# Kernel optimization log

Measured on AMD Instinct MI355X. Metric: run time of the kernel, lower is better.

## Reference

```python
import jax, jax.numpy as jnp
import numpy as np

N_NODES = 50000
N_EDGES = 800000
D_IN = 128
D_HID = 16
N_CLS = 3


def setup_inputs() -> dict:
    key = jax.random.key(0)
    k = jax.random.split(key, 8)
    x = jax.random.normal(k[0], (N_NODES, D_IN), dtype=jnp.float32)
    edge_index = jax.random.randint(k[1], (2, N_EDGES), 0, N_NODES, dtype=jnp.int64)
    # SAGEConv params: lin_l (applied to aggregated neighbors, has bias),
    # lin_r (applied to root node, no bias) -- PyG defaults with mean aggregation.
    s1 = 1.0 / np.sqrt(D_IN)
    s2 = 1.0 / np.sqrt(D_HID)
    W1_l = jax.random.normal(k[2], (D_HID, D_IN), dtype=jnp.float32) * s1
    b1_l = jnp.zeros((D_HID,), dtype=jnp.float32)
    W1_r = jax.random.normal(k[3], (D_HID, D_IN), dtype=jnp.float32) * s1
    W2_l = jax.random.normal(k[4], (N_CLS, D_HID), dtype=jnp.float32) * s2
    b2_l = jnp.zeros((N_CLS,), dtype=jnp.float32)
    W2_r = jax.random.normal(k[5], (N_CLS, D_HID), dtype=jnp.float32) * s2
    return {"x": x, "edge_index": edge_index, "W1_l": W1_l, "b1_l": b1_l,
            "W1_r": W1_r, "W2_l": W2_l, "b2_l": b2_l, "W2_r": W2_r}


def _mean_aggregate(x, src, dst, num_nodes):
    # messages x_j = x[src] scattered to dst, mean-reduced (PyG SAGEConv aggr='mean')
    summed = jax.ops.segment_sum(x[src], dst, num_segments=num_nodes)  # [N, D]
    counts = jax.ops.segment_sum(jnp.ones((src.shape[0],), dtype=x.dtype), dst,
                                 num_segments=num_nodes)
    return summed / jnp.maximum(counts, 1.0)[:, None]


def _sage_conv(x, src, dst, W_l, b_l, W_r, num_nodes):
    agg = _mean_aggregate(x, src, dst, num_nodes)
    return agg @ W_l.T + b_l + x @ W_r.T


def reference(x, edge_index, W1_l, b1_l, W1_r, W2_l, b2_l, W2_r):
    src, dst = edge_index[0], edge_index[1]
    n = x.shape[0]
    h = jax.nn.relu(_sage_conv(x, src, dst, W1_l, b1_l, W1_r, n))
    h = jax.nn.relu(_sage_conv(h, src, dst, W2_l, b2_l, W2_r, n))
    return jax.nn.log_softmax(h, axis=1)
```

## Files before the change

### kernel.cpp

```cpp
#include <hip/hip_runtime.h>
#include <math.h>

#define D_IN 128
#define D_HID 16
#define N_CLS 3
#define NXCD 8

__global__ __launch_bounds__(128) void lin1_kernel(
    const float* __restrict__ x, const float* __restrict__ W1l,
    const float* __restrict__ W1r, float* __restrict__ y_l,
    float* __restrict__ y_r, int n_nodes)
{
    __shared__ float xs[64 * 132];
    __shared__ float ws[32 * 132];
    const int t = threadIdx.x;
    const int node0 = blockIdx.x * 64;

    for (int m = t; m < (32 * 128) / 4; m += 128) {
        int f = m * 4;
        int row = f >> 7, col = f & 127;
        const float* srcw = (row < 16) ? (W1l + row * 128 + col)
                                       : (W1r + (row - 16) * 128 + col);
        float4 g = *(const float4*)srcw;
        *(float4*)&ws[row * 132 + col] = g;
    }
    for (int m = t; m < (64 * 128) / 4; m += 128) {
        int f = m * 4;
        int row = f >> 7, col = f & 127;
        int node = node0 + row;
        float4 g = make_float4(0.f, 0.f, 0.f, 0.f);
        if (node < n_nodes) g = *(const float4*)(x + (size_t)node * D_IN + col);
        *(float4*)&xs[row * 132 + col] = g;
    }
    __syncthreads();

    const int ng = t >> 3;
    const int og = t & 7;
    float acc[4][4];
    #pragma unroll
    for (int i = 0; i < 4; ++i)
        #pragma unroll
        for (int j = 0; j < 4; ++j) acc[i][j] = 0.f;

    for (int k = 0; k < 128; k += 4) {
        float4 xv[4], wv[4];
        #pragma unroll
        for (int i = 0; i < 4; ++i)
            xv[i] = *(const float4*)&xs[(ng + 16 * i) * 132 + k];
        #pragma unroll
        for (int j = 0; j < 4; ++j)
            wv[j] = *(const float4*)&ws[(og + 8 * j) * 132 + k];
        #pragma unroll
        for (int i = 0; i < 4; ++i)
            #pragma unroll
            for (int j = 0; j < 4; ++j) {
                acc[i][j] = fmaf(xv[i].x, wv[j].x, acc[i][j]);
                acc[i][j] = fmaf(xv[i].y, wv[j].y, acc[i][j]);
                acc[i][j] = fmaf(xv[i].z, wv[j].z, acc[i][j]);
                acc[i][j] = fmaf(xv[i].w, wv[j].w, acc[i][j]);
            }
    }

    #pragma unroll
    for (int i = 0; i < 4; ++i) {
        int node = node0 + ng + 16 * i;
        if (node >= n_nodes) continue;
        #pragma unroll
        for (int j = 0; j < 4; ++j) {
            int col = og + 8 * j;
            if (col < 16) y_l[(size_t)node * 16 + col] = acc[i][j];
            else          y_r[(size_t)node * 16 + (col - 16)] = acc[i][j];
        }
    }
}


__global__ __launch_bounds__(256) void fillx_kernel(
    const int* __restrict__ src, const int* __restrict__ dst,
    int* __restrict__ deg, int* __restrict__ padadj,
    int n_edges, int cap, int n8, int n_nodes, int bpx)
{
    const int x  = blockIdx.x & (NXCD - 1);
    const int q  = blockIdx.x >> 3;
    const int lo = x * n8;
    int hi = lo + n8; if (hi > n_nodes) hi = n_nodes;
    const int stride = bpx * 256;

    const int e4n = n_edges >> 2;
    for (int i = q * 256 + threadIdx.x; i < e4n; i += stride) {
        int4 d4 = *(const int4*)&dst[i * 4];
        if (d4.x >= lo && d4.x < hi) {
            int r = atomicAdd(&deg[d4.x], 1);
            if (r < cap) padadj[(size_t)d4.x * cap + r] = src[i * 4 + 0];
        }
        if (d4.y >= lo && d4.y < hi) {
            int r = atomicAdd(&deg[d4.y], 1);
            if (r < cap) padadj[(size_t)d4.y * cap + r] = src[i * 4 + 1];
        }
        if (d4.z >= lo && d4.z < hi) {
            int r = atomicAdd(&deg[d4.z], 1);
            if (r < cap) padadj[(size_t)d4.z * cap + r] = src[i * 4 + 2];
        }
        if (d4.w >= lo && d4.w < hi) {
            int r = atomicAdd(&deg[d4.w], 1);
            if (r < cap) padadj[(size_t)d4.w * cap + r] = src[i * 4 + 3];
        }
    }
    if (q == 0 && threadIdx.x < (n_edges & 3)) {
        int e = (e4n << 2) + threadIdx.x;
        int d = dst[e];
        if (d >= lo && d < hi) {
            int r = atomicAdd(&deg[d], 1);
            if (r < cap) padadj[(size_t)d * cap + r] = src[e];
        }
    }
}

__global__ __launch_bounds__(256) void gather1x_kernel(
    const int* __restrict__ deg, const int* __restrict__ padadj,
    const float* __restrict__ y_l, const float* __restrict__ y_r,
    const float* __restrict__ b1, const float* __restrict__ W2l,
    const float* __restrict__ W2r, float* __restrict__ z_l,
    float* __restrict__ z_r, int n_nodes, int cap, int n8)
{
    const int t = threadIdx.x;
    const int c = t & 15;
    const int x = blockIdx.x & (NXCD - 1);
    const int q = blockIdx.x >> 3;
    const int local = q * 16 + (t >> 4);
    if (local >= n8) return;
    const int n = x * n8 + local;
    if (n >= n_nodes) return;

    const int dc = deg[n];
    const int* ap = padadj + (size_t)n * cap;
    float acc = 0.f;
    int j = 0;
    for (; j + 4 <= dc; j += 4) {
        int4 s4 = *(const int4*)(ap + j);
        float a0 = y_l[(size_t)s4.x * 16 + c];
        float a1 = y_l[(size_t)s4.y * 16 + c];
        float a2 = y_l[(size_t)s4.z * 16 + c];
        float a3 = y_l[(size_t)s4.w * 16 + c];
        acc += (a0 + a1) + (a2 + a3);
    }
    for (; j < dc; ++j) acc += y_l[(size_t)ap[j] * 16 + c];

    float inv = 1.0f / fmaxf((float)dc, 1.0f);
    float h = fmaxf(fmaf(acc, inv, b1[c] + y_r[(size_t)n * 16 + c]), 0.f);

    float zl[N_CLS], zr[N_CLS];
    #pragma unroll
    for (int o = 0; o < N_CLS; ++o) {
        float pl = h * W2l[o * 16 + c];
        float pr = h * W2r[o * 16 + c];
        #pragma unroll
        for (int d = 1; d < 16; d <<= 1) {
            pl += __shfl_xor(pl, d, 64);
            pr += __shfl_xor(pr, d, 64);
        }
        zl[o] = pl; zr[o] = pr;
    }
    if (c == 0) {
        *(float4*)&z_l[(size_t)n * 4] = make_float4(zl[0], zl[1], zl[2], 0.f);
        *(float4*)&z_r[(size_t)n * 4] = make_float4(zr[0], zr[1], zr[2], 0.f);
    }
}

__global__ __launch_bounds__(256) void gather2x_out_kernel(
    const int* __restrict__ deg, const int* __restrict__ padadj,
    const float* __restrict__ z_l, const float* __restrict__ z_r,
    const float* __restrict__ b2, float* __restrict__ out,
    int n_nodes, int cap, int n8)
{
    const int x = blockIdx.x & (NXCD - 1);
    const int q = blockIdx.x >> 3;
    const int local = q * 256 + threadIdx.x;
    if (local >= n8) return;
    const int n = x * n8 + local;
    if (n >= n_nodes) return;

    const int dc = deg[n];
    const int* ap = padadj + (size_t)n * cap;
    float a0 = 0.f, a1 = 0.f, a2 = 0.f;
    int j = 0;
    for (; j + 4 <= dc; j += 4) {
        int4 s4 = *(const int4*)(ap + j);
        float4 v0 = *(const float4*)&z_l[(size_t)s4.x * 4];
        float4 v1 = *(const float4*)&z_l[(size_t)s4.y * 4];
        float4 v2 = *(const float4*)&z_l[(size_t)s4.z * 4];
        float4 v3 = *(const float4*)&z_l[(size_t)s4.w * 4];
        a0 += (v0.x + v1.x) + (v2.x + v3.x);
        a1 += (v0.y + v1.y) + (v2.y + v3.y);
        a2 += (v0.z + v1.z) + (v2.z + v3.z);
    }
    for (; j < dc; ++j) {
        float4 v = *(const float4*)&z_l[(size_t)ap[j] * 4];
        a0 += v.x; a1 += v.y; a2 += v.z;
    }
    float inv = 1.0f / fmaxf((float)dc, 1.0f);
    float4 r = *(const float4*)&z_r[(size_t)n * 4];
    float v0 = fmaxf(fmaf(a0, inv, b2[0] + r.x), 0.f);
    float v1 = fmaxf(fmaf(a1, inv, b2[1] + r.y), 0.f);
    float v2 = fmaxf(fmaf(a2, inv, b2[2] + r.z), 0.f);
    float m = fmaxf(fmaxf(v0, v1), v2);
    float s = expf(v0 - m) + expf(v1 - m) + expf(v2 - m);
    float lse = m + logf(s);
    out[(size_t)n * 3 + 0] = v0 - lse;
    out[(size_t)n * 3 + 1] = v1 - lse;
    out[(size_t)n * 3 + 2] = v2 - lse;
}


__global__ __launch_bounds__(256) void hist_kernel(
    const int* __restrict__ dst, int* __restrict__ deg, int n_edges)
{
    int e = blockIdx.x * 256 + threadIdx.x;
    if (e < n_edges) atomicAdd(&deg[dst[e]], 1);
}

__global__ __launch_bounds__(1024) void scan_a_kernel(
    const int* __restrict__ deg, int* __restrict__ off,
    int* __restrict__ cur, int* __restrict__ bsum, int n)
{
    __shared__ int s[1024];
    const int t = threadIdx.x;
    const int base = blockIdx.x * 4096 + t * 4;
    int4 v = make_int4(0, 0, 0, 0);
    if (base + 3 < n) {
        v = *(const int4*)&deg[base];
    } else {
        if (base + 0 < n) v.x = deg[base + 0];
        if (base + 1 < n) v.y = deg[base + 1];
        if (base + 2 < n) v.z = deg[base + 2];
        if (base + 3 < n) v.w = deg[base + 3];
    }
    int tsum = v.x + v.y + v.z + v.w;
    s[t] = tsum;
    __syncthreads();
    for (int d = 1; d < 1024; d <<= 1) {
        int u = (t >= d) ? s[t - d] : 0;
        __syncthreads();
        s[t] += u;
        __syncthreads();
    }
    if (t == 1023) bsum[blockIdx.x] = s[1023];
    int e0 = s[t] - tsum;
    int e1 = e0 + v.x, e2 = e1 + v.y, e3 = e2 + v.z;
    if (base + 3 < n) {
        *(int4*)&off[base] = make_int4(e0, e1, e2, e3);
        *(int4*)&cur[base] = make_int4(e0, e1, e2, e3);
    } else {
        if (base + 0 < n) { off[base + 0] = e0; cur[base + 0] = e0; }
        if (base + 1 < n) { off[base + 1] = e1; cur[base + 1] = e1; }
        if (base + 2 < n) { off[base + 2] = e2; cur[base + 2] = e2; }
        if (base + 3 < n) { off[base + 3] = e3; cur[base + 3] = e3; }
    }
}

__global__ __launch_bounds__(64) void scan_b_kernel(
    int* __restrict__ bsum, int* __restrict__ off, int nblk, int n)
{
    const int t = threadIdx.x;
    int v = (t < nblk) ? bsum[t] : 0;
    int own = v;
    #pragma unroll
    for (int d = 1; d < 64; d <<= 1) {
        int u = __shfl_up(v, d, 64);
        if (t >= d) v += u;
    }
    if (t < nblk) bsum[t] = v - own;
    if (t == 63) off[n] = v;
}

__global__ __launch_bounds__(256) void scan_c_kernel(
    const int* __restrict__ bsum, int* __restrict__ off,
    int* __restrict__ cur, int n)
{
    int i = blockIdx.x * 256 + threadIdx.x;
    if (i >= n) return;
    int b = bsum[i >> 12];
    off[i] += b;
    cur[i] += b;
}

__global__ __launch_bounds__(256) void fill_kernel(
    const int* __restrict__ src, const int* __restrict__ dst,
    int* __restrict__ cursor, int* __restrict__ adj, int n_edges)
{
    int e = blockIdx.x * 256 + threadIdx.x;
    if (e >= n_edges) return;
    int slot = atomicAdd(&cursor[dst[e]], 1);
    adj[slot] = src[e];
}

__global__ __launch_bounds__(256) void gather1_kernel(
    const int* __restrict__ off, const int* __restrict__ adj,
    const float* __restrict__ y_l, const float* __restrict__ y_r,
    const float* __restrict__ b1, const float* __restrict__ W2l,
    const float* __restrict__ W2r, float* __restrict__ z_l,
    float* __restrict__ z_r, int n_nodes)
{
    const int t = threadIdx.x;
    const int c = t & 15;
    const int n = blockIdx.x * 16 + (t >> 4);
    if (n >= n_nodes) return;
    const int beg = off[n], end = off[n + 1];
    float acc = 0.f;
    for (int j = beg; j < end; ++j) {
        int s = adj[j];
        acc += y_l[(size_t)s * 16 + c];
    }
    float inv = 1.0f / fmaxf((float)(end - beg), 1.0f);
    float h = fmaxf(fmaf(acc, inv, b1[c] + y_r[(size_t)n * 16 + c]), 0.f);

    float zl[N_CLS], zr[N_CLS];
    #pragma unroll
    for (int o = 0; o < N_CLS; ++o) {
        float pl = h * W2l[o * 16 + c];
        float pr = h * W2r[o * 16 + c];
        #pragma unroll
        for (int d = 1; d < 16; d <<= 1) {
            pl += __shfl_xor(pl, d, 64);
            pr += __shfl_xor(pr, d, 64);
        }
        zl[o] = pl; zr[o] = pr;
    }
    if (c == 0) {
        *(float4*)&z_l[(size_t)n * 4] = make_float4(zl[0], zl[1], zl[2], 0.f);
        *(float4*)&z_r[(size_t)n * 4] = make_float4(zr[0], zr[1], zr[2], 0.f);
    }
}

__global__ __launch_bounds__(256) void gather2_out_kernel(
    const int* __restrict__ off, const int* __restrict__ adj,
    const float* __restrict__ z_l, const float* __restrict__ z_r,
    const float* __restrict__ b2, float* __restrict__ out, int n_nodes)
{
    int n = blockIdx.x * 256 + threadIdx.x;
    if (n >= n_nodes) return;
    const int beg = off[n], end = off[n + 1];
    float a0 = 0.f, a1 = 0.f, a2 = 0.f;
    for (int j = beg; j < end; ++j) {
        int s = adj[j];
        float4 v = *(const float4*)&z_l[(size_t)s * 4];
        a0 += v.x; a1 += v.y; a2 += v.z;
    }
    float inv = 1.0f / fmaxf((float)(end - beg), 1.0f);
    float4 r = *(const float4*)&z_r[(size_t)n * 4];
    float v0 = fmaxf(fmaf(a0, inv, b2[0] + r.x), 0.f);
    float v1 = fmaxf(fmaf(a1, inv, b2[1] + r.y), 0.f);
    float v2 = fmaxf(fmaf(a2, inv, b2[2] + r.z), 0.f);
    float m = fmaxf(fmaxf(v0, v1), v2);
    float s = expf(v0 - m) + expf(v1 - m) + expf(v2 - m);
    float lse = m + logf(s);
    out[(size_t)n * 3 + 0] = v0 - lse;
    out[(size_t)n * 3 + 1] = v1 - lse;
    out[(size_t)n * 3 + 2] = v2 - lse;
}

extern "C" void kernel_launch(void* const* d_in, const int* in_sizes, int n_in,
                              void* d_out, int out_size, void* d_ws, size_t ws_size,
                              hipStream_t stream)
{
    const float* x   = (const float*)d_in[0];
    const int*   ei  = (const int*)d_in[1];
    const float* W1l = (const float*)d_in[2];
    const float* b1  = (const float*)d_in[3];
    const float* W1r = (const float*)d_in[4];
    const float* W2l = (const float*)d_in[5];
    const float* b2  = (const float*)d_in[6];
    const float* W2r = (const float*)d_in[7];

    const int N = in_sizes[0] / D_IN;
    const int E = in_sizes[1] / 2;
    const int* srcI = ei;
    const int* dstI = ei + E;

    float* fws  = (float*)d_ws;
    float* y_l  = fws;
    float* y_r  = y_l + (size_t)N * 16;
    float* z_l  = y_r + (size_t)N * 16;
    float* z_r  = z_l + (size_t)N * 4;
    int*   iws  = (int*)(z_r + (size_t)N * 4);

    const size_t base_bytes = 160ULL * N + 4ULL * N;
    int CAP = 0;
    if (ws_size >= base_bytes + 256ULL * N)      CAP = 64;
    else if (ws_size >= base_bytes + 192ULL * N) CAP = 48;

    lin1_kernel<<<(N + 63) / 64, 128, 0, stream>>>(x, W1l, W1r, y_l, y_r, N);

    if (CAP) {
        int* deg    = iws;
        int* padadj = deg + N;
        const int n8  = (N + NXCD - 1) / NXCD;
        const int bpx = 128;

        hipMemsetAsync(deg, 0, (size_t)N * sizeof(int), stream);
        fillx_kernel<<<NXCD * bpx, 256, 0, stream>>>(srcI, dstI, deg, padadj,
                                                     E, CAP, n8, N, bpx);
        const int g1b = (n8 + 15) / 16;
        gather1x_kernel<<<NXCD * g1b, 256, 0, stream>>>(deg, padadj, y_l, y_r,
                                                        b1, W2l, W2r,
                                                        z_l, z_r, N, CAP, n8);
        const int g2b = (n8 + 255) / 256;
        gather2x_out_kernel<<<NXCD * g2b, 256, 0, stream>>>(deg, padadj,
                                                            z_l, z_r, b2,
                                                            (float*)d_out, N, CAP, n8);
    } else {
        int* deg  = iws;
        int* off  = deg + N;
        int* cur  = off + N + 1;
        int* adj  = cur + N;
        int* bsum = adj + E;

        const int nblk = (N + 4095) >> 12;

        hipMemsetAsync(deg, 0, (size_t)N * sizeof(int), stream);
        hist_kernel<<<(E + 255) / 256, 256, 0, stream>>>(dstI, deg, E);
        scan_a_kernel<<<nblk, 1024, 0, stream>>>(deg, off, cur, bsum, N);
        scan_b_kernel<<<1, 64, 0, stream>>>(bsum, off, nblk, N);
        scan_c_kernel<<<(N + 255) / 256, 256, 0, stream>>>(bsum, off, cur, N);
        fill_kernel<<<(E + 255) / 256, 256, 0, stream>>>(srcI, dstI, cur, adj, E);
        gather1_kernel<<<(N + 15) / 16, 256, 0, stream>>>(off, adj, y_l, y_r, b1,
                                                          W2l, W2r, z_l, z_r, N);
        gather2_out_kernel<<<(N + 255) / 256, 256, 0, stream>>>(off, adj, z_l, z_r,
                                                                b2, (float*)d_out, N);
    }
}
```

Baseline: 97.64 us.

## Build CSR via per-block shared-memory histograms and XCD-partitioned placement

Replaces the padded-adjacency default path with an exact CSR build. Each block, partitioned by destination range per XCD, counts edges in a shared-memory histogram, and a column scan gives per-block offsets. Edges are then placed with shared atomics, and the gather kernels read compact CSR with int4-vectorized neighbor loads. This avoids global atomics and padded slots, at the cost of more kernel launches, a CB×N count buffer in workspace, and reading the edge list twice.

After: 98.55 us. About the same (+0.9%).

```diff
diff --git a/kernel.cpp b/kernel.cpp
--- a/kernel.cpp
+++ b/kernel.cpp
@@ -5,6 +5,9 @@
 #define D_HID 16
 #define N_CLS 3
 #define NXCD 8
+#define CB 64
+#define CT 512
+#define HMAX 8192
 
 __global__ __launch_bounds__(128) void lin1_kernel(
     const float* __restrict__ x, const float* __restrict__ W1l,
@@ -72,6 +75,266 @@
             else          y_r[(size_t)node * 16 + (col - 16)] = acc[i][j];
         }
     }
+}
+
+
+__global__ __launch_bounds__(CT) void count_kernel(
+    const int* __restrict__ dst, int* __restrict__ bcnt,
+    int e4n, int n_edges, int n8, int n_nodes, int N)
+{
+    __shared__ int hist[HMAX];
+    const int x = blockIdx.x & (NXCD - 1);
+    const int b = blockIdx.x >> 3;
+    const int lo = x * n8;
+    int hi = lo + n8; if (hi > n_nodes) hi = n_nodes;
+    const int nloc = hi - lo;
+
+    for (int k = threadIdx.x; k < nloc; k += CT) hist[k] = 0;
+    __syncthreads();
+
+    const int g = b * CT + threadIdx.x;
+    const int stride = CB * CT;
+    for (int i = g; i < e4n; i += stride) {
+        int4 d4 = *(const int4*)&dst[i * 4];
+        if (d4.x >= lo && d4.x < hi) atomicAdd(&hist[d4.x - lo], 1);
+        if (d4.y >= lo && d4.y < hi) atomicAdd(&hist[d4.y - lo], 1);
+        if (d4.z >= lo && d4.z < hi) atomicAdd(&hist[d4.z - lo], 1);
+        if (d4.w >= lo && d4.w < hi) atomicAdd(&hist[d4.w - lo], 1);
+    }
+    if (b == 0 && threadIdx.x < (n_edges & 3)) {
+        int e = (e4n << 2) + threadIdx.x;
+        int d = dst[e];
+        if (d >= lo && d < hi) atomicAdd(&hist[d - lo], 1);
+    }
+    __syncthreads();
+    for (int k = threadIdx.x; k < nloc; k += CT)
+        bcnt[(size_t)b * N + lo + k] = hist[k];
+}
+
+__global__ __launch_bounds__(256) void colscan_kernel(
+    int* __restrict__ bcnt, int* __restrict__ deg, int n, int N)
+{
+    int d = blockIdx.x * 256 + threadIdx.x;
+    if (d >= n) return;
+    int s = 0;
+    #pragma unroll 4
+    for (int b = 0; b < CB; ++b) {
+        size_t idx = (size_t)b * N + d;
+        int t = bcnt[idx];
+        bcnt[idx] = s;
+        s += t;
+    }
+    deg[d] = s;
+}
+
+__global__ __launch_bounds__(1024) void scan_a_kernel(
+    const int* __restrict__ deg, int* __restrict__ off,
+    int* __restrict__ bsum, int n)
+{
+    __shared__ int s[1024];
+    const int t = threadIdx.x;
+    const int base = blockIdx.x * 4096 + t * 4;
+    int4 v = make_int4(0, 0, 0, 0);
+    if (base + 3 < n) {
+        v = *(const int4*)&deg[base];
+    } else {
+        if (base + 0 < n) v.x = deg[base + 0];
+        if (base + 1 < n) v.y = deg[base + 1];
+        if (base + 2 < n) v.z = deg[base + 2];
+        if (base + 3 < n) v.w = deg[base + 3];
+    }
+    int tsum = v.x + v.y + v.z + v.w;
+    s[t] = tsum;
+    __syncthreads();
+    for (int d = 1; d < 1024; d <<= 1) {
+        int u = (t >= d) ? s[t - d] : 0;
+        __syncthreads();
+        s[t] += u;
+        __syncthreads();
+    }
+    if (t == 1023) bsum[blockIdx.x] = s[1023];
+    int e0 = s[t] - tsum;
+    int e1 = e0 + v.x, e2 = e1 + v.y, e3 = e2 + v.z;
+    if (base + 3 < n) {
+        *(int4*)&off[base] = make_int4(e0, e1, e2, e3);
+    } else {
+        if (base + 0 < n) off[base + 0] = e0;
+        if (base + 1 < n) off[base + 1] = e1;
+        if (base + 2 < n) off[base + 2] = e2;
+        if (base + 3 < n) off[base + 3] = e3;
+    }
+}
+
+__global__ __launch_bounds__(64) void scan_b_kernel(
+    int* __restrict__ bsum, int* __restrict__ off, int nblk, int n)
+{
+    const int t = threadIdx.x;
+    int v = (t < nblk) ? bsum[t] : 0;
+    int own = v;
+    #pragma unroll
+    for (int d = 1; d < 64; d <<= 1) {
+        int u = __shfl_up(v, d, 64);
+        if (t >= d) v += u;
+    }
+    if (t < nblk) bsum[t] = v - own;
+    if (t == 63) off[n] = v;
+}
+
+__global__ __launch_bounds__(256) void scan_c_kernel(
+    const int* __restrict__ bsum, int* __restrict__ off, int n)
+{
+    int i = blockIdx.x * 256 + threadIdx.x;
+    if (i >= n) return;
+    off[i] += bsum[i >> 12];
+}
+
+__global__ __launch_bounds__(CT) void place_kernel(
+    const int* __restrict__ src, const int* __restrict__ dst,
+    const int* __restrict__ off, const int* __restrict__ bcnt,
+    int* __restrict__ adj, int e4n, int n_edges, int n8, int n_nodes, int N)
+{
+    __shared__ int cur[HMAX];
+    const int x = blockIdx.x & (NXCD - 1);
+    const int b = blockIdx.x >> 3;
+    const int lo = x * n8;
+    int hi = lo + n8; if (hi > n_nodes) hi = n_nodes;
+    const int nloc = hi - lo;
+
+    for (int k = threadIdx.x; k < nloc; k += CT)
+        cur[k] = off[lo + k] + bcnt[(size_t)b * N + lo + k];
+    __syncthreads();
+
+    const int g = b * CT + threadIdx.x;
+    const int stride = CB * CT;
+    for (int i = g; i < e4n; i += stride) {
+        int4 d4 = *(const int4*)&dst[i * 4];
+        if (d4.x >= lo && d4.x < hi) {
+            int p = atomicAdd(&cur[d4.x - lo], 1);
+            adj[p] = src[i * 4 + 0];
+        }
+        if (d4.y >= lo && d4.y < hi) {
+            int p = atomicAdd(&cur[d4.y - lo], 1);
+            adj[p] = src[i * 4 + 1];
+        }
+        if (d4.z >= lo && d4.z < hi) {
+            int p = atomicAdd(&cur[d4.z - lo], 1);
+            adj[p] = src[i * 4 + 2];
+        }
+        if (d4.w >= lo && d4.w < hi) {
+            int p = atomicAdd(&cur[d4.w - lo], 1);
+            adj[p] = src[i * 4 + 3];
+        }
+    }
+    if (b == 0 && threadIdx.x < (n_edges & 3)) {
+        int e = (e4n << 2) + threadIdx.x;
+        int d = dst[e];
+        if (d >= lo && d < hi) {
+            int p = atomicAdd(&cur[d - lo], 1);
+            adj[p] = src[e];
+        }
+    }
+}
+
+__global__ __launch_bounds__(256) void gather1c_kernel(
+    const int* __restrict__ off, const int* __restrict__ adj,
+    const float* __restrict__ y_l, const float* __restrict__ y_r,
+    const float* __restrict__ b1, const float* __restrict__ W2l,
+    const float* __restrict__ W2r, float* __restrict__ z_l,
+    float* __restrict__ z_r, int n_nodes, int n8)
+{
+    const int t = threadIdx.x;
+    const int c = t & 15;
+    const int x = blockIdx.x & (NXCD - 1);
+    const int q = blockIdx.x >> 3;
+    const int local = q * 16 + (t >> 4);
+    if (local >= n8) return;
+    const int n = x * n8 + local;
+    if (n >= n_nodes) return;
+
+    const int beg = off[n], end = off[n + 1];
+    float acc = 0.f;
+    int j = beg;
+    int alim = (beg + 3) & ~3;
+    if (alim > end) alim = end;
+    for (; j < alim; ++j) acc += y_l[(size_t)adj[j] * 16 + c];
+    for (; j + 4 <= end; j += 4) {
+        int4 s4 = *(const int4*)&adj[j];
+        float a0 = y_l[(size_t)s4.x * 16 + c];
+        float a1 = y_l[(size_t)s4.y * 16 + c];
+        float a2 = y_l[(size_t)s4.z * 16 + c];
+        float a3 = y_l[(size_t)s4.w * 16 + c];
+        acc += (a0 + a1) + (a2 + a3);
+    }
+    for (; j < end; ++j) acc += y_l[(size_t)adj[j] * 16 + c];
+
+    float inv = 1.0f / fmaxf((float)(end - beg), 1.0f);
+    float h = fmaxf(fmaf(acc, inv, b1[c] + y_r[(size_t)n * 16 + c]), 0.f);
+
+    float zl[N_CLS], zr[N_CLS];
+    #pragma unroll
+    for (int o = 0; o < N_CLS; ++o) {
+        float pl = h * W2l[o * 16 + c];
+        float pr = h * W2r[o * 16 + c];
+        #pragma unroll
+        for (int d = 1; d < 16; d <<= 1) {
+            pl += __shfl_xor(pl, d, 64);
+            pr += __shfl_xor(pr, d, 64);
+        }
+        zl[o] = pl; zr[o] = pr;
+    }
+    if (c == 0) {
+        *(float4*)&z_l[(size_t)n * 4] = make_float4(zl[0], zl[1], zl[2], 0.f);
+        *(float4*)&z_r[(size_t)n * 4] = make_float4(zr[0], zr[1], zr[2], 0.f);
+    }
+}
+
+__global__ __launch_bounds__(256) void gather2c_out_kernel(
+    const int* __restrict__ off, const int* __restrict__ adj,
+    const float* __restrict__ z_l, const float* __restrict__ z_r,
+    const float* __restrict__ b2, float* __restrict__ out,
+    int n_nodes, int n8)
+{
+    const int x = blockIdx.x & (NXCD - 1);
+    const int q = blockIdx.x >> 3;
+    const int local = q * 256 + threadIdx.x;
+    if (local >= n8) return;
+    const int n = x * n8 + local;
+    if (n >= n_nodes) return;
+
+    const int beg = off[n], end = off[n + 1];
+    float a0 = 0.f, a1 = 0.f, a2 = 0.f;
+    int j = beg;
+    int alim = (beg + 3) & ~3;
+    if (alim > end) alim = end;
+    for (; j < alim; ++j) {
+        float4 v = *(const float4*)&z_l[(size_t)adj[j] * 4];
+        a0 += v.x; a1 += v.y; a2 += v.z;
+    }
+    for (; j + 4 <= end; j += 4) {
+        int4 s4 = *(const int4*)&adj[j];
+        float4 v0 = *(const float4*)&z_l[(size_t)s4.x * 4];
+        float4 v1 = *(const float4*)&z_l[(size_t)s4.y * 4];
+        float4 v2 = *(const float4*)&z_l[(size_t)s4.z * 4];
+        float4 v3 = *(const float4*)&z_l[(size_t)s4.w * 4];
+        a0 += (v0.x + v1.x) + (v2.x + v3.x);
+        a1 += (v0.y + v1.y) + (v2.y + v3.y);
+        a2 += (v0.z + v1.z) + (v2.z + v3.z);
+    }
+    for (; j < end; ++j) {
+        float4 v = *(const float4*)&z_l[(size_t)adj[j] * 4];
+        a0 += v.x; a1 += v.y; a2 += v.z;
+    }
+    float inv = 1.0f / fmaxf((float)(end - beg), 1.0f);
+    float4 r = *(const float4*)&z_r[(size_t)n * 4];
+    float v0 = fmaxf(fmaf(a0, inv, b2[0] + r.x), 0.f);
+    float v1 = fmaxf(fmaf(a1, inv, b2[1] + r.y), 0.f);
+    float v2 = fmaxf(fmaf(a2, inv, b2[2] + r.z), 0.f);
+    float m = fmaxf(fmaxf(v0, v1), v2);
+    float s = expf(v0 - m) + expf(v1 - m) + expf(v2 - m);
+    float lse = m + logf(s);
+    out[(size_t)n * 3 + 0] = v0 - lse;
+    out[(size_t)n * 3 + 1] = v1 - lse;
+    out[(size_t)n * 3 + 2] = v2 - lse;
 }
 
 
@@ -211,154 +474,6 @@
     out[(size_t)n * 3 + 2] = v2 - lse;
 }
 
-
-__global__ __launch_bounds__(256) void hist_kernel(
-    const int* __restrict__ dst, int* __restrict__ deg, int n_edges)
-{
-    int e = blockIdx.x * 256 + threadIdx.x;
-    if (e < n_edges) atomicAdd(&deg[dst[e]], 1);
-}
-
-__global__ __launch_bounds__(1024) void scan_a_kernel(
-    const int* __restrict__ deg, int* __restrict__ off,
-    int* __restrict__ cur, int* __restrict__ bsum, int n)
-{
-    __shared__ int s[1024];
-    const int t = threadIdx.x;
-    const int base = blockIdx.x * 4096 + t * 4;
-    int4 v = make_int4(0, 0, 0, 0);
-    if (base + 3 < n) {
-        v = *(const int4*)&deg[base];
-    } else {
-        if (base + 0 < n) v.x = deg[base + 0];
-        if (base + 1 < n) v.y = deg[base + 1];
-        if (base + 2 < n) v.z = deg[base + 2];
-        if (base + 3 < n) v.w = deg[base + 3];
-    }
-    int tsum = v.x + v.y + v.z + v.w;
-    s[t] = tsum;
-    __syncthreads();
-    for (int d = 1; d < 1024; d <<= 1) {
-        int u = (t >= d) ? s[t - d] : 0;
-        __syncthreads();
-        s[t] += u;
-        __syncthreads();
-    }
-    if (t == 1023) bsum[blockIdx.x] = s[1023];
-    int e0 = s[t] - tsum;
-    int e1 = e0 + v.x, e2 = e1 + v.y, e3 = e2 + v.z;
-    if (base + 3 < n) {
-        *(int4*)&off[base] = make_int4(e0, e1, e2, e3);
-        *(int4*)&cur[base] = make_int4(e0, e1, e2, e3);
-    } else {
-        if (base + 0 < n) { off[base + 0] = e0; cur[base + 0] = e0; }
-        if (base + 1 < n) { off[base + 1] = e1; cur[base + 1] = e1; }
-        if (base + 2 < n) { off[base + 2] = e2; cur[base + 2] = e2; }
-        if (base + 3 < n) { off[base + 3] = e3; cur[base + 3] = e3; }
-    }
-}
-
-__global__ __launch_bounds__(64) void scan_b_kernel(
-    int* __restrict__ bsum, int* __restrict__ off, int nblk, int n)
-{
-    const int t = threadIdx.x;
-    int v = (t < nblk) ? bsum[t] : 0;
-    int own = v;
-    #pragma unroll
-    for (int d = 1; d < 64; d <<= 1) {
-        int u = __shfl_up(v, d, 64);
-        if (t >= d) v += u;
-    }
-    if (t < nblk) bsum[t] = v - own;
-    if (t == 63) off[n] = v;
-}
-
-__global__ __launch_bounds__(256) void scan_c_kernel(
-    const int* __restrict__ bsum, int* __restrict__ off,
-    int* __restrict__ cur, int n)
-{
-    int i = blockIdx.x * 256 + threadIdx.x;
-    if (i >= n) return;
-    int b = bsum[i >> 12];
-    off[i] += b;
-    cur[i] += b;
-}
-
-__global__ __launch_bounds__(256) void fill_kernel(
-    const int* __restrict__ src, const int* __restrict__ dst,
-    int* __restrict__ cursor, int* __restrict__ adj, int n_edges)
-{
-    int e = blockIdx.x * 256 + threadIdx.x;
-    if (e >= n_edges) return;
-    int slot = atomicAdd(&cursor[dst[e]], 1);
-    adj[slot] = src[e];
-}
-
-__global__ __launch_bounds__(256) void gather1_kernel(
-    const int* __restrict__ off, const int* __restrict__ adj,
-    const float* __restrict__ y_l, const float* __restrict__ y_r,
-    const float* __restrict__ b1, const float* __restrict__ W2l,
-    const float* __restrict__ W2r, float* __restrict__ z_l,
-    float* __restrict__ z_r, int n_nodes)
-{
-    const int t = threadIdx.x;
-    const int c = t & 15;
-    const int n = blockIdx.x * 16 + (t >> 4);
-    if (n >= n_nodes) return;
-    const int beg = off[n], end = off[n + 1];
-    float acc = 0.f;
-    for (int j = beg; j < end; ++j) {
-        int s = adj[j];
-        acc += y_l[(size_t)s * 16 + c];
-    }
-    float inv = 1.0f / fmaxf((float)(end - beg), 1.0f);
-    float h = fmaxf(fmaf(acc, inv, b1[c] + y_r[(size_t)n * 16 + c]), 0.f);
-
-    float zl[N_CLS], zr[N_CLS];
-    #pragma unroll
-    for (int o = 0; o < N_CLS; ++o) {
-        float pl = h * W2l[o * 16 + c];
-        float pr = h * W2r[o * 16 + c];
-        #pragma unroll
-        for (int d = 1; d < 16; d <<= 1) {
-            pl += __shfl_xor(pl, d, 64);
-            pr += __shfl_xor(pr, d, 64);
-        }
-        zl[o] = pl; zr[o] = pr;
-    }
-    if (c == 0) {
-        *(float4*)&z_l[(size_t)n * 4] = make_float4(zl[0], zl[1], zl[2], 0.f);
-        *(float4*)&z_r[(size_t)n * 4] = make_float4(zr[0], zr[1], zr[2], 0.f);
-    }
-}
-
-__global__ __launch_bounds__(256) void gather2_out_kernel(
-    const int* __restrict__ off, const int* __restrict__ adj,
-    const float* __restrict__ z_l, const float* __restrict__ z_r,
-    const float* __restrict__ b2, float* __restrict__ out, int n_nodes)
-{
-    int n = blockIdx.x * 256 + threadIdx.x;
-    if (n >= n_nodes) return;
-    const int beg = off[n], end = off[n + 1];
-    float a0 = 0.f, a1 = 0.f, a2 = 0.f;
-    for (int j = beg; j < end; ++j) {
-        int s = adj[j];
-        float4 v = *(const float4*)&z_l[(size_t)s * 4];
-        a0 += v.x; a1 += v.y; a2 += v.z;
-    }
-    float inv = 1.0f / fmaxf((float)(end - beg), 1.0f);
-    float4 r = *(const float4*)&z_r[(size_t)n * 4];
-    float v0 = fmaxf(fmaf(a0, inv, b2[0] + r.x), 0.f);
-    float v1 = fmaxf(fmaf(a1, inv, b2[1] + r.y), 0.f);
-    float v2 = fmaxf(fmaf(a2, inv, b2[2] + r.z), 0.f);
-    float m = fmaxf(fmaxf(v0, v1), v2);
-    float s = expf(v0 - m) + expf(v1 - m) + expf(v2 - m);
-    float lse = m + logf(s);
-    out[(size_t)n * 3 + 0] = v0 - lse;
-    out[(size_t)n * 3 + 1] = v1 - lse;
-    out[(size_t)n * 3 + 2] = v2 - lse;
-}
-
 extern "C" void kernel_launch(void* const* d_in, const int* in_sizes, int n_in,
                               void* d_out, int out_size, void* d_ws, size_t ws_size,
                               hipStream_t stream)
@@ -384,17 +499,43 @@
     float* z_r  = z_l + (size_t)N * 4;
     int*   iws  = (int*)(z_r + (size_t)N * 4);
 
-    const size_t base_bytes = 160ULL * N + 4ULL * N;
-    int CAP = 0;
-    if (ws_size >= base_bytes + 256ULL * N)      CAP = 64;
-    else if (ws_size >= base_bytes + 192ULL * N) CAP = 48;
+    const int n8 = (N + NXCD - 1) / NXCD;
+
+    const size_t need_main = 160ULL * N +
+        4ULL * ((size_t)CB * N + N + (N + 1) + E + 64);
 
     lin1_kernel<<<(N + 63) / 64, 128, 0, stream>>>(x, W1l, W1r, y_l, y_r, N);
 
-    if (CAP) {
+    if (n8 <= HMAX && ws_size >= need_main) {
+        int* bcnt = iws;
+        int* deg  = bcnt + (size_t)CB * N;
+        int* off  = deg + N;
+        int* adj  = off + N + 1;
+        int* bsum = adj + E;
+
+        const int e4n  = E >> 2;
+        const int nblk = (N + 4095) >> 12;
+
+        count_kernel<<<NXCD * CB, CT, 0, stream>>>(dstI, bcnt, e4n, E, n8, N, N);
+        colscan_kernel<<<(N + 255) / 256, 256, 0, stream>>>(bcnt, deg, N, N);
+        scan_a_kernel<<<nblk, 1024, 0, stream>>>(deg, off, bsum, N);
+        scan_b_kernel<<<1, 64, 0, stream>>>(bsum, off, nblk, N);
+        scan_c_kernel<<<(N + 255) / 256, 256, 0, stream>>>(bsum, off, N);
+        place_kernel<<<NXCD * CB, CT, 0, stream>>>(srcI, dstI, off, bcnt, adj,
+                                                   e4n, E, n8, N, N);
+
+        const int g1b = (n8 + 15) / 16;
+        gather1c_kernel<<<NXCD * g1b, 256, 0, stream>>>(off, adj, y_l, y_r, b1,
+                                                        W2l, W2r, z_l, z_r, N, n8);
+        const int g2b = (n8 + 255) / 256;
+        gather2c_out_kernel<<<NXCD * g2b, 256, 0, stream>>>(off, adj, z_l, z_r,
+                                                            b2, (float*)d_out,
+                                                            N, n8);
+    } else {
+        int CAP = 64;
+        if (ws_size < 160ULL * N + 4ULL * N + 256ULL * N) CAP = 48;
         int* deg    = iws;
         int* padadj = deg + N;
-        const int n8  = (N + NXCD - 1) / NXCD;
         const int bpx = 128;
 
         hipMemsetAsync(deg, 0, (size_t)N * sizeof(int), stream);
@@ -408,24 +549,5 @@
         gather2x_out_kernel<<<NXCD * g2b, 256, 0, stream>>>(deg, padadj,
                                                             z_l, z_r, b2,
                                                             (float*)d_out, N, CAP, n8);
-    } else {
-        int* deg  = iws;
-        int* off  = deg + N;
-        int* cur  = off + N + 1;
-        int* adj  = cur + N;
-        int* bsum = adj + E;
-
-        const int nblk = (N + 4095) >> 12;
-
-        hipMemsetAsync(deg, 0, (size_t)N * sizeof(int), stream);
-        hist_kernel<<<(E + 255) / 256, 256, 0, stream>>>(dstI, deg, E);
-        scan_a_kernel<<<nblk, 1024, 0, stream>>>(deg, off, cur, bsum, N);
-        scan_b_kernel<<<1, 64, 0, stream>>>(bsum, off, nblk, N);
-        scan_c_kernel<<<(N + 255) / 256, 256, 0, stream>>>(bsum, off, cur, N);
-        fill_kernel<<<(E + 255) / 256, 256, 0, stream>>>(srcI, dstI, cur, adj, E);
-        gather1_kernel<<<(N + 15) / 16, 256, 0, stream>>>(off, adj, y_l, y_r, b1,
-                                                          W2l, W2r, z_l, z_r, N);
-        gather2_out_kernel<<<(N + 255) / 256, 256, 0, stream>>>(off, adj, z_l, z_r,
-                                                                b2, (float*)d_out, N);
-    }
-}
+    }
+}
```
